# Kernel tuning notes

Hardware: AMD Instinct MI355X
Metric: run time of the kernel (lower is better)

## Reference

```python
import jax, jax.numpy as jnp
import numpy as np

N = 1_048_576   # flattened tokens
C = 128         # classes
IGNORE = 0
GAMMA = 1.0     # FocalLoss bug: alpha default (1) becomes self.gamma
BETA = 1.0      # ClassficationAndMDCA: self.beta = alpha = 1.0


def setup_inputs() -> dict:
    key = jax.random.key(0)
    k1, k2 = jax.random.split(key)
    inputs = jax.random.normal(k1, (N, C), dtype=jnp.float32)
    targets = jax.random.randint(k2, (N,), 0, C, dtype=jnp.int64)
    return {"inputs": inputs, "targets": targets}


def reference(inputs, targets):
    # ignore_index filtering expressed as masked reductions (jit-friendly)
    mask = (targets != IGNORE)
    maskf = mask.astype(inputs.dtype)               # [N]
    nvalid = jnp.sum(maskf)

    # Focal loss: -(1-pt)^gamma * log pt, mean over valid tokens
    logp = jax.nn.log_softmax(inputs, axis=1)       # [N, C]
    logpt = jnp.take_along_axis(logp, targets[:, None], axis=1)[:, 0]  # [N]
    pt = jnp.exp(logpt)
    focal = -((1.0 - pt) ** GAMMA) * logpt
    loss_cls = jnp.sum(focal * maskf) / nvalid

    # MDCA: per-class |mean confidence - mean label frequency|, mean over classes
    probs = jnp.exp(logp)                           # softmax, reuse log_softmax
    avg_conf = jnp.sum(probs * maskf[:, None], axis=0) / nvalid        # [C]
    avg_count = jnp.zeros((C,), inputs.dtype).at[targets].add(maskf) / nvalid  # [C]
    loss_cal = jnp.mean(jnp.abs(avg_conf - avg_count))

    return loss_cls + BETA * loss_cal
```

## Files before the change

kernel.cpp:

```cpp
#include <hip/hip_runtime.h>

#define NC 128
#define BLOCK 256
#define GRID 1024
#define DEPTH 4
#define QBYTES 2048
#define WPB (BLOCK / 64)

typedef float f32x4 __attribute__((ext_vector_type(4)));

__global__ void cmdca_init(float* __restrict__ acc) {
    if (threadIdx.x < 260) acc[threadIdx.x] = 0.0f;
}

template <int CTRL>
__device__ __forceinline__ float dpp_add(float v) {
    int s = __builtin_amdgcn_update_dpp(0, __float_as_int(v), CTRL, 0xF, 0xF, true);
    return v + __int_as_float(s);
}
__device__ __forceinline__ float rowsum16(float v) {
    v = dpp_add<0x121>(v);
    v = dpp_add<0x122>(v);
    v = dpp_add<0x124>(v);
    v = dpp_add<0x128>(v);
    return v;
}

__global__ __launch_bounds__(BLOCK) void cmdca_main(const float* __restrict__ in,
                                                    const int* __restrict__ tgt,
                                                    float* __restrict__ acc,
                                                    int nrows) {
    const int lane = threadIdx.x & 63;
    const int l15  = lane & 15;
    const int sub  = lane >> 4;
    const int wid  = threadIdx.x >> 6;
    const int wave = blockIdx.x * WPB + wid;
    const int nwaves = GRID * WPB;
    const int qtot = nrows >> 2;

    __shared__ char  stage[WPB * DEPTH * QBYTES];
    __shared__ int   tstage[WPB * DEPTH * 64];
    __shared__ float sconf[NC];
    __shared__ float scnt[NC];
    __shared__ float sfn[2];

    char* wstage = stage  + wid * DEPTH * QBYTES;
    int*  wts    = tstage + wid * DEPTH * 64;

    for (int i = threadIdx.x; i < NC; i += BLOCK) { sconf[i] = 0.f; scnt[i] = 0.f; }
    if (threadIdx.x < 2) sfn[threadIdx.x] = 0.f;
    __syncthreads();

    float conf[8] = {0.f, 0.f, 0.f, 0.f, 0.f, 0.f, 0.f, 0.f};
    float focal = 0.f, nval = 0.f;

    const int n = (qtot > wave) ? (qtot - 1 - wave) / nwaves + 1 : 0;

    auto stg = [&](int j, int slot) {
        size_t q = (size_t)wave + (size_t)j * nwaves;
        const char* g = (const char*)in + q * QBYTES + lane * 16;
        __builtin_amdgcn_global_load_lds(
            (const __attribute__((address_space(1))) void*)g,
            (__attribute__((address_space(3))) void*)(wstage + slot * QBYTES),
            16, 0, 0);
        __builtin_amdgcn_global_load_lds(
            (const __attribute__((address_space(1))) void*)(g + 1024),
            (__attribute__((address_space(3))) void*)(wstage + slot * QBYTES + 1024),
            16, 0, 0);
        __builtin_amdgcn_global_load_lds(
            (const __attribute__((address_space(1))) void*)(tgt + 4 * q + (lane & 3)),
            (__attribute__((address_space(3))) void*)(wts + slot * 64),
            4, 0, 0);
    };

    auto cmp = [&](int slot) {
        const char* b = wstage + slot * QBYTES + sub * 512 + l15 * 32;
        f32x4 xa = *(const f32x4*)b;
        f32x4 xb = *(const f32x4*)(b + 16);
        int t = wts[slot * 64 + sub];
        const int te = t & 7;
        float s01 = (te & 1) ? xa.y : xa.x;
        float s23 = (te & 1) ? xa.w : xa.z;
        float s45 = (te & 1) ? xb.y : xb.x;
        float s67 = (te & 1) ? xb.w : xb.z;
        float s03 = (te & 2) ? s23 : s01;
        float s47 = (te & 2) ? s67 : s45;
        float xsel = (te & 4) ? s47 : s03;
        float e0 = __expf(xa.x), e1 = __expf(xa.y), e2 = __expf(xa.z), e3 = __expf(xa.w);
        float e4 = __expf(xb.x), e5 = __expf(xb.y), e6 = __expf(xb.z), e7 = __expf(xb.w);
        float s8 = ((e0 + e1) + (e2 + e3)) + ((e4 + e5) + (e6 + e7));
        float s = rowsum16(s8);
        float invs = __builtin_amdgcn_rcpf(s);
        float logZ = __logf(s);
        int srcl = (lane & 48) | (t >> 3);
        float xt = __int_as_float(
            __builtin_amdgcn_ds_bpermute(srcl << 2, __float_as_int(xsel)));
        float logpt = xt - logZ;
        float pt = __expf(logpt);
        float valid = (t != 0) ? 1.0f : 0.0f;
        float vs = valid * invs;
        conf[0] += vs * e0; conf[1] += vs * e1; conf[2] += vs * e2; conf[3] += vs * e3;
        conf[4] += vs * e4; conf[5] += vs * e5; conf[6] += vs * e6; conf[7] += vs * e7;
        if (l15 == 0) {
            nval  += valid;
            focal += valid * (pt - 1.0f) * logpt;
            if (valid != 0.0f) atomicAdd(&scnt[t], 1.0f);
        }
    };

    for (int jp = 0; jp < n && jp < DEPTH - 1; ++jp) stg(jp, jp);
    int j = 0;
    for (; j + (DEPTH - 1) < n; ++j) {
        stg(j + DEPTH - 1, (j + DEPTH - 1) & (DEPTH - 1));
        asm volatile("s_waitcnt vmcnt(9)" ::: "memory");
        cmp(j & (DEPTH - 1));
    }
    for (; j < n; ++j) {
        int after = n - 1 - j;
        if (after >= 2)      { asm volatile("s_waitcnt vmcnt(6)" ::: "memory"); }
        else if (after == 1) { asm volatile("s_waitcnt vmcnt(3)" ::: "memory"); }
        else                 { asm volatile("s_waitcnt vmcnt(0)" ::: "memory"); }
        cmp(j & (DEPTH - 1));
    }

    __syncthreads();
    const int cb = 8 * l15;
    atomicAdd(&sconf[cb + 0], conf[0]);
    atomicAdd(&sconf[cb + 1], conf[1]);
    atomicAdd(&sconf[cb + 2], conf[2]);
    atomicAdd(&sconf[cb + 3], conf[3]);
    atomicAdd(&sconf[cb + 4], conf[4]);
    atomicAdd(&sconf[cb + 5], conf[5]);
    atomicAdd(&sconf[cb + 6], conf[6]);
    atomicAdd(&sconf[cb + 7], conf[7]);
    if (l15 == 0) {
        atomicAdd(&sfn[0], focal);
        atomicAdd(&sfn[1], nval);
    }
    __syncthreads();
    if (threadIdx.x < NC) {
        atomicAdd(&acc[threadIdx.x],      sconf[threadIdx.x]);
        atomicAdd(&acc[NC + threadIdx.x], scnt[threadIdx.x]);
    }
    if (threadIdx.x == 0) {
        atomicAdd(&acc[2 * NC],     sfn[0]);
        atomicAdd(&acc[2 * NC + 1], sfn[1]);
    }
}

__global__ void cmdca_fin(const float* __restrict__ acc, float* __restrict__ out) {
    int c = threadIdx.x;
    float nvalid = acc[2 * NC + 1];
    float diff = fabsf(acc[c] - acc[NC + c]) / nvalid;
    #pragma unroll
    for (int o = 32; o; o >>= 1) diff += __shfl_xor(diff, o);
    __shared__ float sh[2];
    if ((threadIdx.x & 63) == 0) sh[threadIdx.x >> 6] = diff;
    __syncthreads();
    if (threadIdx.x == 0) {
        float loss_cal = (sh[0] + sh[1]) / (float)NC;
        float loss_cls = acc[2 * NC] / nvalid;
        out[0] = loss_cls + loss_cal;
    }
}

extern "C" void kernel_launch(void* const* d_in, const int* in_sizes, int n_in,
                              void* d_out, int out_size, void* d_ws, size_t ws_size,
                              hipStream_t stream) {
    const float* in  = (const float*)d_in[0];
    const int*   tgt = (const int*)d_in[1];
    float* out = (float*)d_out;
    float* acc = (float*)d_ws;
    int nrows = in_sizes[0] / NC;

    hipLaunchKernelGGL(cmdca_init, dim3(1), dim3(512), 0, stream, acc);
    hipLaunchKernelGGL(cmdca_main, dim3(GRID), dim3(BLOCK), 0, stream, in, tgt, acc, nrows);
    hipLaunchKernelGGL(cmdca_fin,  dim3(1), dim3(NC), 0, stream, acc, out);
}
```

Baseline: 117.7 us.

## Split row chunks between LDS-async staging and register-prefetched direct loads

Even iterations keep using the global_load_lds staging ring, while odd iterations are prefetched straight into registers via vector global loads, with four register slots rotating alongside the four LDS slots. This roughly doubles the bytes in flight per wave without growing LDS use, aiming to hide HBM latency better in this bandwidth-bound reduction. It costs extra registers (four RQ structs), which may lower occupancy. The hand-written vmcnt waits now depend on the compiler's ordering of the mixed loads, and the tail uses a simpler non-pipelined path.

```diff
diff --git a/kernel.cpp b/kernel.cpp
--- a/kernel.cpp
+++ b/kernel.cpp
@@ -3,7 +3,6 @@
 #define NC 128
 #define BLOCK 256
 #define GRID 1024
-#define DEPTH 4
 #define QBYTES 2048
 #define WPB (BLOCK / 64)
 
@@ -25,6 +24,8 @@
     v = dpp_add<0x128>(v);
     return v;
 }
+
+struct RQ { f32x4 a, b; int t; };
 
 __global__ __launch_bounds__(BLOCK) void cmdca_main(const float* __restrict__ in,
                                                     const int* __restrict__ tgt,
@@ -38,14 +39,14 @@
     const int nwaves = GRID * WPB;
     const int qtot = nrows >> 2;
 
-    __shared__ char  stage[WPB * DEPTH * QBYTES];
-    __shared__ int   tstage[WPB * DEPTH * 64];
+    __shared__ char  stage[WPB * 4 * QBYTES];
+    __shared__ int   tstage[WPB * 4 * 64];
     __shared__ float sconf[NC];
     __shared__ float scnt[NC];
     __shared__ float sfn[2];
 
-    char* wstage = stage  + wid * DEPTH * QBYTES;
-    int*  wts    = tstage + wid * DEPTH * 64;
+    char* wstage = stage  + wid * 4 * QBYTES;
+    int*  wts    = tstage + wid * 4 * 64;
 
     for (int i = threadIdx.x; i < NC; i += BLOCK) { sconf[i] = 0.f; scnt[i] = 0.f; }
     if (threadIdx.x < 2) sfn[threadIdx.x] = 0.f;
@@ -54,30 +55,7 @@
     float conf[8] = {0.f, 0.f, 0.f, 0.f, 0.f, 0.f, 0.f, 0.f};
     float focal = 0.f, nval = 0.f;
 
-    const int n = (qtot > wave) ? (qtot - 1 - wave) / nwaves + 1 : 0;
-
-    auto stg = [&](int j, int slot) {
-        size_t q = (size_t)wave + (size_t)j * nwaves;
-        const char* g = (const char*)in + q * QBYTES + lane * 16;
-        __builtin_amdgcn_global_load_lds(
-            (const __attribute__((address_space(1))) void*)g,
-            (__attribute__((address_space(3))) void*)(wstage + slot * QBYTES),
-            16, 0, 0);
-        __builtin_amdgcn_global_load_lds(
-            (const __attribute__((address_space(1))) void*)(g + 1024),
-            (__attribute__((address_space(3))) void*)(wstage + slot * QBYTES + 1024),
-            16, 0, 0);
-        __builtin_amdgcn_global_load_lds(
-            (const __attribute__((address_space(1))) void*)(tgt + 4 * q + (lane & 3)),
-            (__attribute__((address_space(3))) void*)(wts + slot * 64),
-            4, 0, 0);
-    };
-
-    auto cmp = [&](int slot) {
-        const char* b = wstage + slot * QBYTES + sub * 512 + l15 * 32;
-        f32x4 xa = *(const f32x4*)b;
-        f32x4 xb = *(const f32x4*)(b + 16);
-        int t = wts[slot * 64 + sub];
+    auto cmpv = [&](f32x4 xa, f32x4 xb, int t) {
         const int te = t & 7;
         float s01 = (te & 1) ? xa.y : xa.x;
         float s23 = (te & 1) ? xa.w : xa.z;
@@ -108,20 +86,76 @@
         }
     };
 
-    for (int jp = 0; jp < n && jp < DEPTH - 1; ++jp) stg(jp, jp);
-    int j = 0;
-    for (; j + (DEPTH - 1) < n; ++j) {
-        stg(j + DEPTH - 1, (j + DEPTH - 1) & (DEPTH - 1));
-        asm volatile("s_waitcnt vmcnt(9)" ::: "memory");
-        cmp(j & (DEPTH - 1));
-    }
-    for (; j < n; ++j) {
-        int after = n - 1 - j;
-        if (after >= 2)      { asm volatile("s_waitcnt vmcnt(6)" ::: "memory"); }
-        else if (after == 1) { asm volatile("s_waitcnt vmcnt(3)" ::: "memory"); }
-        else                 { asm volatile("s_waitcnt vmcnt(0)" ::: "memory"); }
-        cmp(j & (DEPTH - 1));
-    }
+    auto stgL = [&](int p, int slot) {
+        size_t q = (size_t)wave + (size_t)(2 * p) * nwaves;
+        const char* g = (const char*)in + q * QBYTES + lane * 16;
+        __builtin_amdgcn_global_load_lds(
+            (const __attribute__((address_space(1))) void*)g,
+            (__attribute__((address_space(3))) void*)(wstage + slot * QBYTES),
+            16, 0, 0);
+        __builtin_amdgcn_global_load_lds(
+            (const __attribute__((address_space(1))) void*)(g + 1024),
+            (__attribute__((address_space(3))) void*)(wstage + slot * QBYTES + 1024),
+            16, 0, 0);
+        __builtin_amdgcn_global_load_lds(
+            (const __attribute__((address_space(1))) void*)(tgt + 4 * q + (lane & 3)),
+            (__attribute__((address_space(3))) void*)(wts + slot * 64),
+            4, 0, 0);
+    };
+    auto cmpL = [&](int slot) {
+        const char* b = wstage + slot * QBYTES + sub * 512 + l15 * 32;
+        f32x4 xa = *(const f32x4*)b;
+        f32x4 xb = *(const f32x4*)(b + 16);
+        int t = wts[slot * 64 + sub];
+        cmpv(xa, xb, t);
+    };
+
+    auto ldR = [&](RQ& d, int p) {
+        size_t q = (size_t)wave + (size_t)(2 * p + 1) * nwaves;
+        const float* pr = in + ((q << 2) + sub) * (size_t)NC + l15 * 8;
+        d.a = *reinterpret_cast<const f32x4*>(pr);
+        d.b = *reinterpret_cast<const f32x4*>(pr + 4);
+        d.t = tgt[(q << 2) + sub];
+    };
+
+    auto direct = [&](int j) {
+        size_t q = (size_t)wave + (size_t)j * nwaves;
+        const float* pr = in + ((q << 2) + sub) * (size_t)NC + l15 * 8;
+        f32x4 xa = *reinterpret_cast<const f32x4*>(pr);
+        f32x4 xb = *reinterpret_cast<const f32x4*>(pr + 4);
+        int t = tgt[(q << 2) + sub];
+        cmpv(xa, xb, t);
+    };
+
+    const int n = (qtot > wave) ? (qtot - 1 - wave) / nwaves + 1 : 0;
+    const int m = n >> 1;
+    RQ A, B, C, Dq;
+
+    if (m > 0) { stgL(0, 0); ldR(A, 0); }
+    if (m > 1) { stgL(1, 1); ldR(B, 1); }
+    if (m > 2) { stgL(2, 2); ldR(C, 2); }
+
+    int k = 0;
+    for (; k + 7 <= m; k += 4) {
+        stgL(k + 3, 3); ldR(Dq, k + 3);
+        asm volatile("s_waitcnt vmcnt(18)" ::: "memory");
+        cmpL(0); cmpv(A.a, A.b, A.t);
+        stgL(k + 4, 0); ldR(A, k + 4);
+        asm volatile("s_waitcnt vmcnt(18)" ::: "memory");
+        cmpL(1); cmpv(B.a, B.b, B.t);
+        stgL(k + 5, 1); ldR(B, k + 5);
+        asm volatile("s_waitcnt vmcnt(18)" ::: "memory");
+        cmpL(2); cmpv(C.a, C.b, C.t);
+        stgL(k + 6, 2); ldR(C, k + 6);
+        asm volatile("s_waitcnt vmcnt(18)" ::: "memory");
+        cmpL(3); cmpv(Dq.a, Dq.b, Dq.t);
+    }
+    asm volatile("s_waitcnt vmcnt(0)" ::: "memory");
+    if (k + 0 < m) { cmpL(0); cmpv(A.a, A.b, A.t); }
+    if (k + 1 < m) { cmpL(1); cmpv(B.a, B.b, B.t); }
+    if (k + 2 < m) { cmpL(2); cmpv(C.a, C.b, C.t); }
+    for (int j = k + 3; j < m; ++j) { direct(2 * j); direct(2 * j + 1); }
+    if (n & 1) direct(n - 1);
 
     __syncthreads();
     const int cb = 8 * l15;
```

New measurement: 124.2 us. 5.5% more time.

## Deepen LDS pipeline to five stages with register target loads and wraparound indexing

Applied to the files above, without the earlier changes.

Changes the launch to 768 blocks of 320 threads and deepens the per-wave LDS staging ring to five slots. The loop is unrolled by five and its tail removed: out-of-range quads wrap around and are masked invalid. Targets now come from registers via a plain global load instead of an LDS staging slot. The aim is to keep more loads in flight and drop tail-loop branching, at the cost of extra redundant loads. The fixed vmcnt(12) waits rely on the compiler emitting exactly the expected number of memory ops.

```diff
diff --git a/kernel.cpp b/kernel.cpp
--- a/kernel.cpp
+++ b/kernel.cpp
@@ -1,9 +1,9 @@
 #include <hip/hip_runtime.h>
 
 #define NC 128
-#define BLOCK 256
-#define GRID 1024
-#define DEPTH 4
+#define BLOCK 320
+#define GRID 768
+#define DEPTH 5
 #define QBYTES 2048
 #define WPB (BLOCK / 64)
 
@@ -37,15 +37,15 @@
     const int wave = blockIdx.x * WPB + wid;
     const int nwaves = GRID * WPB;
     const int qtot = nrows >> 2;
+    const int n  = (qtot + nwaves - 1) / nwaves;
+    const int n5 = ((n + 4) / 5) * 5;
 
     __shared__ char  stage[WPB * DEPTH * QBYTES];
-    __shared__ int   tstage[WPB * DEPTH * 64];
     __shared__ float sconf[NC];
     __shared__ float scnt[NC];
     __shared__ float sfn[2];
 
-    char* wstage = stage  + wid * DEPTH * QBYTES;
-    int*  wts    = tstage + wid * DEPTH * 64;
+    char* wstage = stage + wid * DEPTH * QBYTES;
 
     for (int i = threadIdx.x; i < NC; i += BLOCK) { sconf[i] = 0.f; scnt[i] = 0.f; }
     if (threadIdx.x < 2) sfn[threadIdx.x] = 0.f;
@@ -54,11 +54,10 @@
     float conf[8] = {0.f, 0.f, 0.f, 0.f, 0.f, 0.f, 0.f, 0.f};
     float focal = 0.f, nval = 0.f;
 
-    const int n = (qtot > wave) ? (qtot - 1 - wave) / nwaves + 1 : 0;
-
-    auto stg = [&](int j, int slot) {
-        size_t q = (size_t)wave + (size_t)j * nwaves;
-        const char* g = (const char*)in + q * QBYTES + lane * 16;
+    auto stg = [&](int jj, int slot) {
+        int q = wave + jj * nwaves;
+        if (q >= qtot) q -= qtot;
+        const char* g = (const char*)in + (size_t)q * QBYTES + lane * 16;
         __builtin_amdgcn_global_load_lds(
             (const __attribute__((address_space(1))) void*)g,
             (__attribute__((address_space(3))) void*)(wstage + slot * QBYTES),
@@ -67,17 +66,17 @@
             (const __attribute__((address_space(1))) void*)(g + 1024),
             (__attribute__((address_space(3))) void*)(wstage + slot * QBYTES + 1024),
             16, 0, 0);
-        __builtin_amdgcn_global_load_lds(
-            (const __attribute__((address_space(1))) void*)(tgt + 4 * q + (lane & 3)),
-            (__attribute__((address_space(3))) void*)(wts + slot * 64),
-            4, 0, 0);
+    };
+    auto tld = [&](int jj) -> int {
+        int q = wave + jj * nwaves;
+        if (q >= qtot) q -= qtot;
+        return tgt[(q << 2) + sub];
     };
 
-    auto cmp = [&](int slot) {
+    auto cmp = [&](int slot, int t, int jj) {
         const char* b = wstage + slot * QBYTES + sub * 512 + l15 * 32;
         f32x4 xa = *(const f32x4*)b;
         f32x4 xb = *(const f32x4*)(b + 16);
-        int t = wts[slot * 64 + sub];
         const int te = t & 7;
         float s01 = (te & 1) ? xa.y : xa.x;
         float s23 = (te & 1) ? xa.w : xa.z;
@@ -97,7 +96,8 @@
             __builtin_amdgcn_ds_bpermute(srcl << 2, __float_as_int(xsel)));
         float logpt = xt - logZ;
         float pt = __expf(logpt);
-        float valid = (t != 0) ? 1.0f : 0.0f;
+        bool ok = (wave + jj * nwaves) < qtot;
+        float valid = (t != 0 && ok) ? 1.0f : 0.0f;
         float vs = valid * invs;
         conf[0] += vs * e0; conf[1] += vs * e1; conf[2] += vs * e2; conf[3] += vs * e3;
         conf[4] += vs * e4; conf[5] += vs * e5; conf[6] += vs * e6; conf[7] += vs * e7;
@@ -108,19 +108,28 @@
         }
     };
 
-    for (int jp = 0; jp < n && jp < DEPTH - 1; ++jp) stg(jp, jp);
-    int j = 0;
-    for (; j + (DEPTH - 1) < n; ++j) {
-        stg(j + DEPTH - 1, (j + DEPTH - 1) & (DEPTH - 1));
-        asm volatile("s_waitcnt vmcnt(9)" ::: "memory");
-        cmp(j & (DEPTH - 1));
-    }
-    for (; j < n; ++j) {
-        int after = n - 1 - j;
-        if (after >= 2)      { asm volatile("s_waitcnt vmcnt(6)" ::: "memory"); }
-        else if (after == 1) { asm volatile("s_waitcnt vmcnt(3)" ::: "memory"); }
-        else                 { asm volatile("s_waitcnt vmcnt(0)" ::: "memory"); }
-        cmp(j & (DEPTH - 1));
+    int t0, t1, t2, t3, t4;
+    stg(0, 0); t0 = tld(0);
+    stg(1, 1); t1 = tld(1);
+    stg(2, 2); t2 = tld(2);
+    stg(3, 3); t3 = tld(3);
+
+    for (int j = 0; j < n5; j += 5) {
+        stg(j + 4, 4); t4 = tld(j + 4);
+        asm volatile("s_waitcnt vmcnt(12)" ::: "memory");
+        cmp(0, t0, j + 0);
+        stg(j + 5, 0); t0 = tld(j + 5);
+        asm volatile("s_waitcnt vmcnt(12)" ::: "memory");
+        cmp(1, t1, j + 1);
+        stg(j + 6, 1); t1 = tld(j + 6);
+        asm volatile("s_waitcnt vmcnt(12)" ::: "memory");
+        cmp(2, t2, j + 2);
+        stg(j + 7, 2); t2 = tld(j + 7);
+        asm volatile("s_waitcnt vmcnt(12)" ::: "memory");
+        cmp(3, t3, j + 3);
+        stg(j + 8, 3); t3 = tld(j + 8);
+        asm volatile("s_waitcnt vmcnt(12)" ::: "memory");
+        cmp(4, t4, j + 4);
     }
 
     __syncthreads();
```

After: 149.2 us. 1.27x slower.

## Give each wave a contiguous chunk and add a prefetch stream ahead of staging

Applied to the files above, without the earlier changes.

Each wave now handles a contiguous range of quads instead of strided ones, and the main loop is unrolled by two. A lightweight global_load_lds prefetch touches data PD quads ahead, warming cache/DRAM pages for later staging loads. A direct-load fallback covers remainder quads and small per-wave counts. The goal is better DRAM locality and higher memory-level parallelism, at the cost of extra load instructions and changed vmcnt bookkeeping that must stay correct.

```diff
diff --git a/kernel.cpp b/kernel.cpp
--- a/kernel.cpp
+++ b/kernel.cpp
@@ -6,6 +6,7 @@
 #define DEPTH 4
 #define QBYTES 2048
 #define WPB (BLOCK / 64)
+#define PD 4
 
 typedef float f32x4 __attribute__((ext_vector_type(4)));
 
@@ -34,18 +35,23 @@
     const int l15  = lane & 15;
     const int sub  = lane >> 4;
     const int wid  = threadIdx.x >> 6;
-    const int wave = blockIdx.x * WPB + wid;
+    const int w    = blockIdx.x * WPB + wid;
     const int nwaves = GRID * WPB;
     const int qtot = nrows >> 2;
+    const int qpw  = qtot / nwaves;
+    const int rem  = qtot - qpw * nwaves;
+    const size_t qb = (size_t)w * qpw;
 
     __shared__ char  stage[WPB * DEPTH * QBYTES];
     __shared__ int   tstage[WPB * DEPTH * 64];
+    __shared__ int   pfd[WPB * 64];
     __shared__ float sconf[NC];
     __shared__ float scnt[NC];
     __shared__ float sfn[2];
 
     char* wstage = stage  + wid * DEPTH * QBYTES;
     int*  wts    = tstage + wid * DEPTH * 64;
+    int*  wpfd   = pfd    + wid * 64;
 
     for (int i = threadIdx.x; i < NC; i += BLOCK) { sconf[i] = 0.f; scnt[i] = 0.f; }
     if (threadIdx.x < 2) sfn[threadIdx.x] = 0.f;
@@ -54,30 +60,7 @@
     float conf[8] = {0.f, 0.f, 0.f, 0.f, 0.f, 0.f, 0.f, 0.f};
     float focal = 0.f, nval = 0.f;
 
-    const int n = (qtot > wave) ? (qtot - 1 - wave) / nwaves + 1 : 0;
-
-    auto stg = [&](int j, int slot) {
-        size_t q = (size_t)wave + (size_t)j * nwaves;
-        const char* g = (const char*)in + q * QBYTES + lane * 16;
-        __builtin_amdgcn_global_load_lds(
-            (const __attribute__((address_space(1))) void*)g,
-            (__attribute__((address_space(3))) void*)(wstage + slot * QBYTES),
-            16, 0, 0);
-        __builtin_amdgcn_global_load_lds(
-            (const __attribute__((address_space(1))) void*)(g + 1024),
-            (__attribute__((address_space(3))) void*)(wstage + slot * QBYTES + 1024),
-            16, 0, 0);
-        __builtin_amdgcn_global_load_lds(
-            (const __attribute__((address_space(1))) void*)(tgt + 4 * q + (lane & 3)),
-            (__attribute__((address_space(3))) void*)(wts + slot * 64),
-            4, 0, 0);
-    };
-
-    auto cmp = [&](int slot) {
-        const char* b = wstage + slot * QBYTES + sub * 512 + l15 * 32;
-        f32x4 xa = *(const f32x4*)b;
-        f32x4 xb = *(const f32x4*)(b + 16);
-        int t = wts[slot * 64 + sub];
+    auto cmpv = [&](f32x4 xa, f32x4 xb, int t) {
         const int te = t & 7;
         float s01 = (te & 1) ? xa.y : xa.x;
         float s23 = (te & 1) ? xa.w : xa.z;
@@ -108,20 +91,72 @@
         }
     };
 
-    for (int jp = 0; jp < n && jp < DEPTH - 1; ++jp) stg(jp, jp);
-    int j = 0;
-    for (; j + (DEPTH - 1) < n; ++j) {
-        stg(j + DEPTH - 1, (j + DEPTH - 1) & (DEPTH - 1));
-        asm volatile("s_waitcnt vmcnt(9)" ::: "memory");
-        cmp(j & (DEPTH - 1));
-    }
-    for (; j < n; ++j) {
-        int after = n - 1 - j;
-        if (after >= 2)      { asm volatile("s_waitcnt vmcnt(6)" ::: "memory"); }
-        else if (after == 1) { asm volatile("s_waitcnt vmcnt(3)" ::: "memory"); }
-        else                 { asm volatile("s_waitcnt vmcnt(0)" ::: "memory"); }
-        cmp(j & (DEPTH - 1));
-    }
+    auto stg = [&](int j, int slot) {
+        size_t q = qb + (size_t)j;
+        const char* g = (const char*)in + q * QBYTES + lane * 16;
+        __builtin_amdgcn_global_load_lds(
+            (const __attribute__((address_space(1))) void*)g,
+            (__attribute__((address_space(3))) void*)(wstage + slot * QBYTES),
+            16, 0, 0);
+        __builtin_amdgcn_global_load_lds(
+            (const __attribute__((address_space(1))) void*)(g + 1024),
+            (__attribute__((address_space(3))) void*)(wstage + slot * QBYTES + 1024),
+            16, 0, 0);
+        __builtin_amdgcn_global_load_lds(
+            (const __attribute__((address_space(1))) void*)(tgt + 4 * q + (lane & 3)),
+            (__attribute__((address_space(3))) void*)(wts + slot * 64),
+            4, 0, 0);
+    };
+
+    auto pf = [&](int j) {
+        int qf = j + PD;
+        if (qf > qpw - 2) qf = (qpw >= 2) ? qpw - 2 : 0;
+        const char* g = (const char*)in + (qb + (size_t)qf) * QBYTES + lane * 64;
+        __builtin_amdgcn_global_load_lds(
+            (const __attribute__((address_space(1))) void*)g,
+            (__attribute__((address_space(3))) void*)wpfd,
+            4, 0, 0);
+    };
+
+    auto cmp = [&](int slot) {
+        const char* b = wstage + slot * QBYTES + sub * 512 + l15 * 32;
+        f32x4 xa = *(const f32x4*)b;
+        f32x4 xb = *(const f32x4*)(b + 16);
+        int t = wts[slot * 64 + sub];
+        cmpv(xa, xb, t);
+    };
+
+    auto direct = [&](size_t q) {
+        const float* pr = in + ((q << 2) + sub) * (size_t)NC + l15 * 8;
+        f32x4 xa = *reinterpret_cast<const f32x4*>(pr);
+        f32x4 xb = *reinterpret_cast<const f32x4*>(pr + 4);
+        int t = tgt[(q << 2) + sub];
+        cmpv(xa, xb, t);
+    };
+
+    if (qpw >= 8) {
+        stg(0, 0); stg(1, 1); stg(2, 2); pf(-2);
+        int j = 0;
+        for (; j + 4 < qpw; j += 2) {
+            pf(j);
+            stg(j + 3, (j + 3) & 3);
+            asm volatile("s_waitcnt vmcnt(11)" ::: "memory");
+            cmp(j & 3);
+            stg(j + 4, (j + 4) & 3);
+            asm volatile("s_waitcnt vmcnt(10)" ::: "memory");
+            cmp((j + 1) & 3);
+        }
+        for (; j + 3 < qpw; ++j) {
+            stg(j + 3, (j + 3) & 3);
+            asm volatile("s_waitcnt vmcnt(10)" ::: "memory");
+            cmp(j & 3);
+        }
+        asm volatile("s_waitcnt vmcnt(0)" ::: "memory");
+        for (; j < qpw; ++j) cmp(j & 3);
+    } else {
+        for (int j = 0; j < qpw; ++j) direct(qb + j);
+    }
+    if (w < rem) direct((size_t)qpw * nwaves + w);
 
     __syncthreads();
     const int cb = 8 * l15;
```

Result: slower. 148.6 us (+26.2%).
